# Optimization experiments

Hardware: AMD Instinct MI355X
Metric: run time of the kernel (lower is better)

## Reference

```python
import jax, jax.numpy as jnp
import numpy as np

B, C, H, W = 16, 512, 32, 32
CQ = C // 8  # 64
EPS = 1e-5


def _conv1x1(x, Wt, b=None):
    # x: (B,C,H,W), Wt: (O,C) -> (B,O,H,W)
    y = jnp.einsum('bchw,oc->bohw', x, Wt)
    if b is not None:
        y = y + b[None, :, None, None]
    return y


def setup_inputs() -> dict:
    key = jax.random.key(0)
    ks = jax.random.split(key, 12)
    s = 0.02
    return {
        'rgb':    jax.random.normal(ks[0], (B, C, H, W), jnp.float32),
        'depth':  jax.random.normal(ks[1], (B, C, H, W), jnp.float32),
        'Wq_rgb': jax.random.normal(ks[2], (CQ, C), jnp.float32) * s,
        'bq_rgb': jnp.zeros((CQ,), jnp.float32),
        'Wk_dep': jax.random.normal(ks[3], (CQ, C), jnp.float32) * s,
        'bk_dep': jnp.zeros((CQ,), jnp.float32),
        'Wv_dep': jax.random.normal(ks[4], (C, C), jnp.float32) * s,
        'bv_dep': jnp.zeros((C,), jnp.float32),
        'Wq_dep': jax.random.normal(ks[5], (CQ, C), jnp.float32) * s,
        'bq_dep': jnp.zeros((CQ,), jnp.float32),
        'Wk_rgb': jax.random.normal(ks[6], (CQ, C), jnp.float32) * s,
        'bk_rgb': jnp.zeros((CQ,), jnp.float32),
        'Wv_rgb': jax.random.normal(ks[7], (C, C), jnp.float32) * s,
        'bv_rgb': jnp.zeros((C,), jnp.float32),
        'W_fuse': jax.random.normal(ks[8], (C, 2 * C), jnp.float32) * s,
        'gamma':  jnp.ones((C,), jnp.float32),
        'beta':   jnp.zeros((C,), jnp.float32),
    }


def reference(rgb, depth, Wq_rgb, bq_rgb, Wk_dep, bk_dep, Wv_dep, bv_dep,
              Wq_dep, bq_dep, Wk_rgb, bk_rgb, Wv_rgb, bv_rgb, W_fuse, gamma, beta):
    b, c, h, w = rgb.shape
    hw = h * w
    scale = jnp.asarray(c, rgb.dtype) ** 0.5  # note: full C, as in source

    # RGB attends to depth
    q = _conv1x1(rgb, Wq_rgb, bq_rgb).reshape(b, -1, hw).transpose(0, 2, 1)   # (B,HW,CQ)
    k = _conv1x1(depth, Wk_dep, bk_dep).reshape(b, -1, hw)                    # (B,CQ,HW)
    v = _conv1x1(depth, Wv_dep, bv_dep).reshape(b, -1, hw).transpose(0, 2, 1) # (B,HW,C)
    attn = jax.nn.softmax(jnp.einsum('bnd,bdm->bnm', q, k) / scale, axis=-1)
    rgb_att = jnp.einsum('bnm,bmc->bnc', attn, v).transpose(0, 2, 1).reshape(b, c, h, w)

    # Depth attends to RGB
    q2 = _conv1x1(depth, Wq_dep, bq_dep).reshape(b, -1, hw).transpose(0, 2, 1)
    k2 = _conv1x1(rgb, Wk_rgb, bk_rgb).reshape(b, -1, hw)
    v2 = _conv1x1(rgb, Wv_rgb, bv_rgb).reshape(b, -1, hw).transpose(0, 2, 1)
    attn2 = jax.nn.softmax(jnp.einsum('bnd,bdm->bnm', q2, k2) / scale, axis=-1)
    dep_att = jnp.einsum('bnm,bmc->bnc', attn2, v2).transpose(0, 2, 1).reshape(b, c, h, w)

    cat = jnp.concatenate([rgb_att, dep_att], axis=1)      # (B,2C,H,W)
    fused = jnp.einsum('bchw,oc->bohw', cat, W_fuse)        # 1x1 conv, no bias

    # BatchNorm2d in training mode (batch statistics, biased variance)
    mean = fused.mean(axis=(0, 2, 3))
    var = fused.var(axis=(0, 2, 3))
    normed = (fused - mean[None, :, None, None]) * jax.lax.rsqrt(var + EPS)[None, :, None, None]
    out = normed * gamma[None, :, None, None] + beta[None, :, None, None]
    return jax.nn.relu(out)
```

## Files before the change

kernel.cpp:

```cpp
#include <hip/hip_runtime.h>
#include <math.h>

#define NB 16
#define CC 512
#define CQ 64
#define HWN 1024

typedef float4 f4;
typedef __bf16 bf16x8 __attribute__((ext_vector_type(8)));
typedef float f32x4 __attribute__((ext_vector_type(4)));
typedef __attribute__((ext_vector_type(8))) unsigned short ushort8v;

__device__ __forceinline__ unsigned short f2bf(float f) {
    unsigned int u = __float_as_uint(f);
    u = (u + 0x7fffu + ((u >> 16) & 1u)) >> 16;
    return (unsigned short)u;
}
__device__ __forceinline__ float bf2f(unsigned short u) {
    return __uint_as_float(((unsigned int)u) << 16);
}

__device__ __forceinline__ void gload16(const unsigned short* g, unsigned short* l) {
    __builtin_amdgcn_global_load_lds(
        (const __attribute__((address_space(1))) unsigned int*)g,
        (__attribute__((address_space(3))) unsigned int*)l,
        16, 0, 0);
}

template<int BM, int BN, int BIAS, bool OBF16, int ZSH, bool STATS>
__global__ __launch_bounds__(256)
void mfma_g(const unsigned short* __restrict__ A, long sAlo, long sAhi, int lda,
            const unsigned short* __restrict__ B, long sBlo, long sBhi, int ldb,
            const float* __restrict__ bias, long sBiasHi,
            void* __restrict__ Cout, long sClo, long sChi, int ldc,
            int Ksize, float alpha, float* __restrict__ statsAcc)
{
    constexpr int MF = BM / 32;
    constexpr int NF = BN / 32;
    constexpr int CA = BM / 32;
    constexpr int CB = BN / 32;
    __shared__ unsigned short As[2][BM * 64];
    __shared__ unsigned short Bs[2][BN * 64];

    const int gx = gridDim.x, gy = gridDim.y;
    int f = blockIdx.x + gx * (blockIdx.y + gy * blockIdx.z);
    const int nwg = gx * gy * gridDim.z;
    f = (f & 7) * (nwg >> 3) + (f >> 3);
    const int bx = f % gx; const int t2 = f / gx;
    const int by = t2 % gy; const int bz = t2 / gy;

    const int zlo = ZSH ? (bz & ((1 << ZSH) - 1)) : 0;
    const int zhi = bz >> ZSH;

    const int t = threadIdx.x, lane = t & 63, wid = t >> 6;
    const int wm = (wid >> 1) * (BM / 2), wn = (wid & 1) * (BN / 2);
    const int m0 = by * BM, n0 = bx * BN;
    const unsigned short* Ab = A + (long)zlo * sAlo + (long)zhi * sAhi;
    const unsigned short* Bb = B + (long)zlo * sBlo + (long)zhi * sBhi;

    const int srow = lane >> 3;
    const int scol = ((lane & 7) ^ srow) << 3;
    const unsigned short* gA[CA]; const unsigned short* gB[CB];
    unsigned short* lA[CA]; unsigned short* lB[CB];
#pragma unroll
    for (int c = 0; c < CA; ++c) {
        const int seg = wid + 4 * c;
        gA[c] = Ab + (long)(m0 + seg * 8 + srow) * lda + scol;
        lA[c] = &As[0][seg * 512];
    }
#pragma unroll
    for (int c = 0; c < CB; ++c) {
        const int seg = wid + 4 * c;
        gB[c] = Bb + (long)(n0 + seg * 8 + srow) * ldb + scol;
        lB[c] = &Bs[0][seg * 512];
    }

    f32x4 acc[MF][NF] = {};
    const int l15 = lane & 15, slot = lane >> 4;

#pragma unroll
    for (int c = 0; c < CA; ++c) gload16(gA[c], lA[c]);
#pragma unroll
    for (int c = 0; c < CB; ++c) gload16(gB[c], lB[c]);
    __syncthreads();

    const int nt = Ksize >> 6;
    int cur = 0;
    for (int tt = 0; tt < nt; ++tt) {
        if (tt + 1 < nt) {
            const int ko = (tt + 1) << 6;
            const int nb = cur ^ 1;
#pragma unroll
            for (int c = 0; c < CA; ++c) gload16(gA[c] + ko, lA[c] + nb * (BM * 64));
#pragma unroll
            for (int c = 0; c < CB; ++c) gload16(gB[c] + ko, lB[c] + nb * (BN * 64));
        }
        bf16x8 alo[MF], ahi[MF], blo[NF], bhi[NF];
#pragma unroll
        for (int i = 0; i < MF; ++i) {
            const int r = wm + i * 16 + l15;
            alo[i] = *(const bf16x8*)&As[cur][r * 64 + ((slot ^ (r & 7)) << 3)];
            ahi[i] = *(const bf16x8*)&As[cur][r * 64 + (((slot + 4) ^ (r & 7)) << 3)];
        }
#pragma unroll
        for (int j = 0; j < NF; ++j) {
            const int r = wn + j * 16 + l15;
            blo[j] = *(const bf16x8*)&Bs[cur][r * 64 + ((slot ^ (r & 7)) << 3)];
            bhi[j] = *(const bf16x8*)&Bs[cur][r * 64 + (((slot + 4) ^ (r & 7)) << 3)];
        }
#pragma unroll
        for (int i = 0; i < MF; ++i)
#pragma unroll
            for (int j = 0; j < NF; ++j) {
                acc[i][j] = __builtin_amdgcn_mfma_f32_16x16x32_bf16(alo[i], blo[j], acc[i][j], 0, 0, 0);
                acc[i][j] = __builtin_amdgcn_mfma_f32_16x16x32_bf16(ahi[i], bhi[j], acc[i][j], 0, 0, 0);
            }
        __syncthreads();
        cur ^= 1;
    }

    unsigned short* C16 = (unsigned short*)Cout + (long)zlo * sClo + (long)zhi * sChi;
    float*          C32 = (float*)Cout + (long)zlo * sClo + (long)zhi * sChi;
    const float* biasb = (BIAS != 0) ? bias + (long)zhi * sBiasHi : nullptr;
    const int r0 = slot << 2;
#pragma unroll
    for (int i = 0; i < MF; ++i) {
#pragma unroll
        for (int r = 0; r < 4; ++r) {
            const int m = m0 + wm + i * 16 + r0 + r;
            const float brow = (BIAS == 1) ? biasb[m] : 0.0f;
            float ps = 0.0f, ps2 = 0.0f;
#pragma unroll
            for (int j = 0; j < NF; ++j) {
                const int n = n0 + wn + j * 16 + l15;
                const float bb = (BIAS == 2) ? biasb[n] : brow;
                const float o = alpha * (acc[i][j][r] + bb);
                if (OBF16) C16[(long)m * ldc + n] = f2bf(o);
                else       C32[(long)m * ldc + n] = o;
                if (STATS) { ps += o; ps2 += o * o; }
            }
            if (STATS) {
#pragma unroll
                for (int off = 8; off; off >>= 1) {
                    ps  += __shfl_xor(ps, off);
                    ps2 += __shfl_xor(ps2, off);
                }
                if (l15 == 0) {
                    const int slot2 = ((zlo * gx + bx) << 1) + (wid & 1);
                    statsAcc[(long)m * 256 + slot2]          = ps;
                    statsAcc[131072 + (long)m * 256 + slot2] = ps2;
                }
            }
        }
    }
}

__global__ __launch_bounds__(256)
void attn_fused2(const unsigned short* __restrict__ QK, unsigned short* __restrict__ Pcat)
{
    __shared__ unsigned short Es[16 * 1024];
    const int t = threadIdx.x, lane = t & 63, w = t >> 6;
    const int bx = blockIdx.x, b = blockIdx.y, dir = blockIdx.z;
    const unsigned short* Q = QK + (long)(dir ? b : 16 + b) * 131072;
    const unsigned short* K = QK + (long)(dir ? 16 + b : b) * 131072 + 64;
    const int l15 = lane & 15, slot = lane >> 4, kg = slot << 3;

    const long mrow = (long)bx * 16 + l15;
    bf16x8 aq0 = *(const bf16x8*)&Q[mrow * 128 + kg];
    bf16x8 aq1 = *(const bf16x8*)&Q[mrow * 128 + 32 + kg];

    const int colbase = w << 8;
    const int rbase = slot << 2;
#pragma unroll
    for (int c = 0; c < 4; ++c) {
        const int n0 = colbase + (c << 6);
        bf16x8 bk0[4], bk1[4];
#pragma unroll
        for (int j = 0; j < 4; ++j) {
            const long krow = n0 + (j << 4) + l15;
            bk0[j] = *(const bf16x8*)&K[krow * 128 + kg];
            bk1[j] = *(const bf16x8*)&K[krow * 128 + 32 + kg];
        }
#pragma unroll
        for (int j = 0; j < 4; ++j) {
            f32x4 a = {0.f, 0.f, 0.f, 0.f};
            a = __builtin_amdgcn_mfma_f32_16x16x32_bf16(aq0, bk0[j], a, 0, 0, 0);
            a = __builtin_amdgcn_mfma_f32_16x16x32_bf16(aq1, bk1[j], a, 0, 0, 0);
            const int col = n0 + (j << 4) + l15;
#pragma unroll
            for (int r = 0; r < 4; ++r) {
                const int row = rbase + r;
                Es[(row << 10) + (col ^ (row << 3))] = f2bf(__expf(a[r]));
            }
        }
    }
    __syncthreads();

#pragma unroll
    for (int rr = 0; rr < 4; ++rr) {
        const int R = (w << 2) + rr;
        const int base = R << 10, sw = R << 3;
        const int c8 = lane << 3;
        ushort8v u0 = *(const ushort8v*)&Es[base + (c8 ^ sw)];
        ushort8v u1 = *(const ushort8v*)&Es[base + ((c8 + 512) ^ sw)];
        float v[16];
#pragma unroll
        for (int i = 0; i < 8; ++i) { v[i] = bf2f(u0[i]); v[8 + i] = bf2f(u1[i]); }
        float s = 0.0f;
#pragma unroll
        for (int i = 0; i < 16; ++i) s += v[i];
#pragma unroll
        for (int off = 32; off; off >>= 1) s += __shfl_xor(s, off);
        const float inv = 1.0f / s;
        ushort8v o0, o1;
#pragma unroll
        for (int i = 0; i < 8; ++i) { o0[i] = f2bf(v[i] * inv); o1[i] = f2bf(v[8 + i] * inv); }
        unsigned short* dst = Pcat + ((long)(b * 1024 + bx * 16 + R)) * 2048
                            + dir * 1024 + c8;
        *(ushort8v*)dst = o0;
        *(ushort8v*)(dst + 512) = o1;
    }
}

__global__ __launch_bounds__(256)
void transpose_cvt2(const float* __restrict__ src_dep, const float* __restrict__ src_rgb,
                    unsigned short* __restrict__ dst)
{
    __shared__ float tile[64][65];
    const int t = threadIdx.x;
    const int z = blockIdx.z;
    const float* s = (z < 16 ? src_dep : src_rgb) + (long)(z & 15) * 524288;
    unsigned short* d = dst + (long)z * 524288;
    const int c0 = blockIdx.x << 6, r0 = blockIdx.y << 6;
    const int lr = t >> 4, lc = (t & 15) << 2;
#pragma unroll
    for (int i = 0; i < 4; ++i) {
        f4 v = *(const f4*)(s + (long)(r0 + lr + i * 16) * HWN + c0 + lc);
        *(f4*)&tile[lr + i * 16][lc] = v;
    }
    __syncthreads();
#pragma unroll
    for (int i = 0; i < 4; ++i) {
        const int crow = lr + i * 16;
        ushort4 o;
        o.x = f2bf(tile[lc + 0][crow]);
        o.y = f2bf(tile[lc + 1][crow]);
        o.z = f2bf(tile[lc + 2][crow]);
        o.w = f2bf(tile[lc + 3][crow]);
        *(ushort4*)&d[(long)(c0 + crow) * CC + r0 + lc] = o;
    }
}

__global__ __launch_bounds__(256)
void transpose_cvt(const float* __restrict__ src, unsigned short* __restrict__ dst,
                   int R, int Cn)
{
    __shared__ float tile[64][65];
    const int t = threadIdx.x;
    const int c0 = blockIdx.x << 6, r0 = blockIdx.y << 6;
    const int lr = t >> 4, lc = (t & 15) << 2;
#pragma unroll
    for (int i = 0; i < 4; ++i) {
        f4 v = *(const f4*)(src + (long)(r0 + lr + i * 16) * Cn + c0 + lc);
        *(f4*)&tile[lr + i * 16][lc] = v;
    }
    __syncthreads();
#pragma unroll
    for (int i = 0; i < 4; ++i) {
        const int crow = lr + i * 16;
        ushort4 o;
        o.x = f2bf(tile[lc + 0][crow]);
        o.y = f2bf(tile[lc + 1][crow]);
        o.z = f2bf(tile[lc + 2][crow]);
        o.w = f2bf(tile[lc + 3][crow]);
        *(ushort4*)&dst[(long)(c0 + crow) * R + r0 + lc] = o;
    }
}

__global__ __launch_bounds__(256)
void cvt_flat(const float* __restrict__ src, unsigned short* __restrict__ dst, int n4)
{
    const int i = blockIdx.x * 256 + threadIdx.x;
    if (i < n4) {
        f4 v = ((const f4*)src)[i];
        ushort4 o;
        o.x = f2bf(v.x); o.y = f2bf(v.y); o.z = f2bf(v.z); o.w = f2bf(v.w);
        ((ushort4*)dst)[i] = o;
    }
}

__global__ __launch_bounds__(256)
void prep_wqk(const float* __restrict__ wqd, const float* __restrict__ wkd,
              const float* __restrict__ wqr, const float* __restrict__ wkr,
              unsigned short* __restrict__ dst, float s)
{
    const int i4 = blockIdx.x * 256 + threadIdx.x;
    const int row = i4 >> 7;
    const int seg = row >> 6;
    const float* src = (seg == 0) ? wqd : (seg == 1) ? wkd : (seg == 2) ? wqr : wkr;
    const float sc = (seg & 1) ? 1.0f : s;
    f4 v = ((const f4*)src)[((row & 63) << 7) + (i4 & 127)];
    ushort4 o;
    o.x = f2bf(v.x * sc); o.y = f2bf(v.y * sc); o.z = f2bf(v.z * sc); o.w = f2bf(v.w * sc);
    ((ushort4*)dst)[i4] = o;
}

__global__ __launch_bounds__(256)
void prep_bias(const float* __restrict__ bqd, const float* __restrict__ bkd,
               const float* __restrict__ bqr, const float* __restrict__ bkr,
               float* __restrict__ dst, float s)
{
    const int t = threadIdx.x;
    float v;
    if (t < 64)       v = bqd[t] * s;
    else if (t < 128) v = bkd[t - 64];
    else if (t < 192) v = bqr[t - 128] * s;
    else              v = bkr[t - 192];
    dst[t] = v;
}

__global__ __launch_bounds__(256)
void bfuse_k(const float* __restrict__ Wf, const float* __restrict__ bv1,
             const float* __restrict__ bv2, float* __restrict__ bfuse)
{
    const int o = blockIdx.x, t = threadIdx.x;
    const float* row = Wf + (long)o * 1024;
    float s = row[t] * bv1[t] + row[512 + t] * bv2[t]
            + row[256 + t] * bv1[256 + t] + row[768 + t] * bv2[256 + t];
#pragma unroll
    for (int off = 32; off; off >>= 1) s += __shfl_xor(s, off);
    __shared__ float r[4];
    if ((t & 63) == 0) r[t >> 6] = s;
    __syncthreads();
    if (t == 0) bfuse[o] = r[0] + r[1] + r[2] + r[3];
}

__global__ __launch_bounds__(256)
void bn_finalize(const float* __restrict__ part, float* __restrict__ stats)
{
    const int c = blockIdx.x, t = threadIdx.x;
    float s1 = part[(long)c * 256 + t];
    float s2 = part[131072 + (long)c * 256 + t];
#pragma unroll
    for (int off = 32; off; off >>= 1) {
        s1 += __shfl_xor(s1, off);
        s2 += __shfl_xor(s2, off);
    }
    __shared__ float r1[4], r2[4];
    if ((t & 63) == 0) { r1[t >> 6] = s1; r2[t >> 6] = s2; }
    __syncthreads();
    if (t == 0) {
        const float S1 = r1[0] + r1[1] + r1[2] + r1[3];
        const float S2 = r2[0] + r2[1] + r2[2] + r2[3];
        const float mean = S1 * (1.0f / 16384.0f);
        const float var  = S2 * (1.0f / 16384.0f) - mean * mean;
        stats[c]      = mean;
        stats[CC + c] = rsqrtf(var + 1e-5f);
    }
}

__global__ __launch_bounds__(256)
void bn_apply(const float* __restrict__ fused, const float* __restrict__ stats,
              const float* __restrict__ gamma, const float* __restrict__ beta,
              float* __restrict__ out)
{
    const long i4 = (long)blockIdx.x * 256 + threadIdx.x;
    f4 v = ((const f4*)fused)[i4];
    const int o = (int)((i4 >> 8) & 511);
    const float is = stats[CC + o];
    const float g  = gamma[o] * is;
    const float bb = beta[o] - stats[o] * g;
    v.x = fmaxf(fmaf(v.x, g, bb), 0.0f);
    v.y = fmaxf(fmaf(v.y, g, bb), 0.0f);
    v.z = fmaxf(fmaf(v.z, g, bb), 0.0f);
    v.w = fmaxf(fmaf(v.w, g, bb), 0.0f);
    ((f4*)out)[i4] = v;
}

static constexpr long B_depT  = 0;
static constexpr long B_rgbT  = 16777216;
static constexpr long B_WvT1  = 33554432;
static constexpr long B_WvT2  = 34078720;
static constexpr long B_Wfb   = 34603008;
static constexpr long B_Wqk   = 35651584;
static constexpr long B_Wc1   = 35913728;
static constexpr long B_bfu   = 36962304;
static constexpr long B_bias  = 36964352;
static constexpr long B_QK    = 36966400;
static constexpr long B_Acat  = 45355008;
static constexpr long B_Pcat  = 78909440;
static constexpr long B_fused = 146018304;
static constexpr long B_stats = 179572736;
static constexpr long B_part  = 179576832;

extern "C" void kernel_launch(void* const* d_in, const int* in_sizes, int n_in,
                              void* d_out, int out_size, void* d_ws, size_t ws_size,
                              hipStream_t stream)
{
    const float* rgb    = (const float*)d_in[0];
    const float* depth  = (const float*)d_in[1];
    const float* Wq_rgb = (const float*)d_in[2];
    const float* bq_rgb = (const float*)d_in[3];
    const float* Wk_dep = (const float*)d_in[4];
    const float* bk_dep = (const float*)d_in[5];
    const float* Wv_dep = (const float*)d_in[6];
    const float* bv_dep = (const float*)d_in[7];
    const float* Wq_dep = (const float*)d_in[8];
    const float* bq_dep = (const float*)d_in[9];
    const float* Wk_rgb = (const float*)d_in[10];
    const float* bk_rgb = (const float*)d_in[11];
    const float* Wv_rgb = (const float*)d_in[12];
    const float* bv_rgb = (const float*)d_in[13];
    const float* W_fuse = (const float*)d_in[14];
    const float* gamma  = (const float*)d_in[15];
    const float* beta   = (const float*)d_in[16];
    char* ws = (char*)d_ws;
    float* out = (float*)d_out;

    const float inv_scale = 0.044194173824159223f;
    dim3 blk(256);

    unsigned short* depT = (unsigned short*)(ws + B_depT);
    unsigned short* WvT1 = (unsigned short*)(ws + B_WvT1);
    unsigned short* WvT2 = (unsigned short*)(ws + B_WvT2);
    unsigned short* Wfb  = (unsigned short*)(ws + B_Wfb);
    unsigned short* Wqk  = (unsigned short*)(ws + B_Wqk);
    unsigned short* Wc1  = (unsigned short*)(ws + B_Wc1);
    float*          bfu  = (float*)(ws + B_bfu);
    float*          bias = (float*)(ws + B_bias);
    unsigned short* QK   = (unsigned short*)(ws + B_QK);
    unsigned short* Acat = (unsigned short*)(ws + B_Acat);
    unsigned short* Pcat = (unsigned short*)(ws + B_Pcat);
    float*          fused= (float*)(ws + B_fused);
    float*          stats= (float*)(ws + B_stats);
    float*          part = (float*)(ws + B_part);

    transpose_cvt2<<<dim3(16, 8, 32), blk, 0, stream>>>(depth, rgb, depT);
    transpose_cvt<<<dim3(8, 8, 1), blk, 0, stream>>>(Wv_dep, WvT1, CC, CC);
    transpose_cvt<<<dim3(8, 8, 1), blk, 0, stream>>>(Wv_rgb, WvT2, CC, CC);
    cvt_flat<<<512, blk, 0, stream>>>(W_fuse, Wfb, 131072);
    prep_wqk<<<128, blk, 0, stream>>>(Wq_dep, Wk_dep, Wq_rgb, Wk_rgb, Wqk, inv_scale);
    prep_bias<<<1, blk, 0, stream>>>(bq_dep, bk_dep, bq_rgb, bk_rgb, bias, inv_scale);
    bfuse_k<<<512, blk, 0, stream>>>(W_fuse, bv_dep, bv_rgb, bfu);

    mfma_g<128, 128, 0, true, 0, false><<<dim3(4, 4, 2), blk, 0, stream>>>(
        Wfb, 0, 512, 1024, WvT1, 0, 262144, 512, nullptr, 0,
        Wc1, 0, 262144, 512, 512, 1.0f, nullptr);

    mfma_g<128, 64, 2, true, 4, false><<<dim3(2, 8, 32), blk, 0, stream>>>(
        depT, 524288, 8388608, 512, Wqk, 0, 65536, 512, bias, 128,
        QK, 131072, 2097152, 128, 512, 1.0f, nullptr);

    mfma_g<128, 128, 0, true, 4, false><<<dim3(8, 4, 32), blk, 0, stream>>>(
        Wc1, 0, 262144, 512, depT, 524288, 8388608, 512, nullptr, 0,
        Acat, 1048576, 1024, 2048, 512, 1.0f, nullptr);

    attn_fused2<<<dim3(64, NB, 2), blk, 0, stream>>>(QK, Pcat);

    mfma_g<128, 128, 1, false, 4, true><<<dim3(8, 4, 16), blk, 0, stream>>>(
        Acat, 1048576, 0, 2048, Pcat, 2097152, 0, 2048, bfu, 0,
        fused, 524288, 0, 1024, 2048, 1.0f, part);

    bn_finalize<<<512, blk, 0, stream>>>(part, stats);
    bn_apply<<<8192, blk, 0, stream>>>(fused, stats, gamma, beta, out);
}
```

Baseline: 175.5 us.

## Store fused output as bf16, merge weight transposes, remap attention blocks, widen QK tile

The fused 1x1-conv output is now written in bf16 instead of fp32, and the BN apply kernel reads it as bf16. This halves the traffic for that intermediate write and read. The two Wv transposes become one launch, the attention grid is remapped so consecutive blocks are spread across XCD-like groups, and the QK projection GEMM uses a 128-wide N tile. BN statistics still come from the fp32 partial sums, but the normalized values are computed from bf16-rounded data, which adds precision error.

```diff
diff --git a/kernel.cpp b/kernel.cpp
--- a/kernel.cpp
+++ b/kernel.cpp
@@ -160,7 +160,9 @@
 {
     __shared__ unsigned short Es[16 * 1024];
     const int t = threadIdx.x, lane = t & 63, w = t >> 6;
-    const int bx = blockIdx.x, b = blockIdx.y, dir = blockIdx.z;
+    int p = blockIdx.x + 64 * (blockIdx.y + 16 * blockIdx.z);
+    p = (p & 7) * 256 + (p >> 3);
+    const int bx = p & 63, b = (p >> 6) & 15, dir = p >> 10;
     const unsigned short* Q = QK + (long)(dir ? b : 16 + b) * 131072;
     const unsigned short* K = QK + (long)(dir ? 16 + b : b) * 131072 + 64;
     const int l15 = lane & 15, slot = lane >> 4, kg = slot << 3;
@@ -252,16 +254,19 @@
 }
 
 __global__ __launch_bounds__(256)
-void transpose_cvt(const float* __restrict__ src, unsigned short* __restrict__ dst,
-                   int R, int Cn)
+void transpose_cvtW(const float* __restrict__ w0, const float* __restrict__ w1,
+                    unsigned short* __restrict__ dst)
 {
     __shared__ float tile[64][65];
     const int t = threadIdx.x;
+    const int z = blockIdx.z;
+    const float* src = z ? w1 : w0;
+    unsigned short* d = dst + (long)z * 262144;
     const int c0 = blockIdx.x << 6, r0 = blockIdx.y << 6;
     const int lr = t >> 4, lc = (t & 15) << 2;
 #pragma unroll
     for (int i = 0; i < 4; ++i) {
-        f4 v = *(const f4*)(src + (long)(r0 + lr + i * 16) * Cn + c0 + lc);
+        f4 v = *(const f4*)(src + (long)(r0 + lr + i * 16) * CC + c0 + lc);
         *(f4*)&tile[lr + i * 16][lc] = v;
     }
     __syncthreads();
@@ -273,7 +278,7 @@
         o.y = f2bf(tile[lc + 1][crow]);
         o.z = f2bf(tile[lc + 2][crow]);
         o.w = f2bf(tile[lc + 3][crow]);
-        *(ushort4*)&dst[(long)(c0 + crow) * R + r0 + lc] = o;
+        *(ushort4*)&d[(long)(c0 + crow) * CC + r0 + lc] = o;
     }
 }
 
@@ -360,27 +365,32 @@
 }
 
 __global__ __launch_bounds__(256)
-void bn_apply(const float* __restrict__ fused, const float* __restrict__ stats,
-              const float* __restrict__ gamma, const float* __restrict__ beta,
-              float* __restrict__ out)
-{
-    const long i4 = (long)blockIdx.x * 256 + threadIdx.x;
-    f4 v = ((const f4*)fused)[i4];
-    const int o = (int)((i4 >> 8) & 511);
+void bn_apply_bf16(const unsigned short* __restrict__ fused, const float* __restrict__ stats,
+                   const float* __restrict__ gamma, const float* __restrict__ beta,
+                   float* __restrict__ out)
+{
+    const long i8 = (long)blockIdx.x * 256 + threadIdx.x;
+    ushort8v v = ((const ushort8v*)fused)[i8];
+    const int o = (int)((i8 >> 7) & 511);
     const float is = stats[CC + o];
     const float g  = gamma[o] * is;
     const float bb = beta[o] - stats[o] * g;
-    v.x = fmaxf(fmaf(v.x, g, bb), 0.0f);
-    v.y = fmaxf(fmaf(v.y, g, bb), 0.0f);
-    v.z = fmaxf(fmaf(v.z, g, bb), 0.0f);
-    v.w = fmaxf(fmaf(v.w, g, bb), 0.0f);
-    ((f4*)out)[i4] = v;
+    f4 o0, o1;
+    o0.x = fmaxf(fmaf(bf2f(v[0]), g, bb), 0.0f);
+    o0.y = fmaxf(fmaf(bf2f(v[1]), g, bb), 0.0f);
+    o0.z = fmaxf(fmaf(bf2f(v[2]), g, bb), 0.0f);
+    o0.w = fmaxf(fmaf(bf2f(v[3]), g, bb), 0.0f);
+    o1.x = fmaxf(fmaf(bf2f(v[4]), g, bb), 0.0f);
+    o1.y = fmaxf(fmaf(bf2f(v[5]), g, bb), 0.0f);
+    o1.z = fmaxf(fmaf(bf2f(v[6]), g, bb), 0.0f);
+    o1.w = fmaxf(fmaf(bf2f(v[7]), g, bb), 0.0f);
+    ((f4*)out)[i8 * 2]     = o0;
+    ((f4*)out)[i8 * 2 + 1] = o1;
 }
 
 static constexpr long B_depT  = 0;
 static constexpr long B_rgbT  = 16777216;
 static constexpr long B_WvT1  = 33554432;
-static constexpr long B_WvT2  = 34078720;
 static constexpr long B_Wfb   = 34603008;
 static constexpr long B_Wqk   = 35651584;
 static constexpr long B_Wc1   = 35913728;
@@ -422,7 +432,6 @@
 
     unsigned short* depT = (unsigned short*)(ws + B_depT);
     unsigned short* WvT1 = (unsigned short*)(ws + B_WvT1);
-    unsigned short* WvT2 = (unsigned short*)(ws + B_WvT2);
     unsigned short* Wfb  = (unsigned short*)(ws + B_Wfb);
     unsigned short* Wqk  = (unsigned short*)(ws + B_Wqk);
     unsigned short* Wc1  = (unsigned short*)(ws + B_Wc1);
@@ -431,13 +440,12 @@
     unsigned short* QK   = (unsigned short*)(ws + B_QK);
     unsigned short* Acat = (unsigned short*)(ws + B_Acat);
     unsigned short* Pcat = (unsigned short*)(ws + B_Pcat);
-    float*          fused= (float*)(ws + B_fused);
+    unsigned short* fused= (unsigned short*)(ws + B_fused);
     float*          stats= (float*)(ws + B_stats);
     float*          part = (float*)(ws + B_part);
 
     transpose_cvt2<<<dim3(16, 8, 32), blk, 0, stream>>>(depth, rgb, depT);
-    transpose_cvt<<<dim3(8, 8, 1), blk, 0, stream>>>(Wv_dep, WvT1, CC, CC);
-    transpose_cvt<<<dim3(8, 8, 1), blk, 0, stream>>>(Wv_rgb, WvT2, CC, CC);
+    transpose_cvtW<<<dim3(8, 8, 2), blk, 0, stream>>>(Wv_dep, Wv_rgb, WvT1);
     cvt_flat<<<512, blk, 0, stream>>>(W_fuse, Wfb, 131072);
     prep_wqk<<<128, blk, 0, stream>>>(Wq_dep, Wk_dep, Wq_rgb, Wk_rgb, Wqk, inv_scale);
     prep_bias<<<1, blk, 0, stream>>>(bq_dep, bk_dep, bq_rgb, bk_rgb, bias, inv_scale);
@@ -447,7 +455,7 @@
         Wfb, 0, 512, 1024, WvT1, 0, 262144, 512, nullptr, 0,
         Wc1, 0, 262144, 512, 512, 1.0f, nullptr);
 
-    mfma_g<128, 64, 2, true, 4, false><<<dim3(2, 8, 32), blk, 0, stream>>>(
+    mfma_g<128, 128, 2, true, 4, false><<<dim3(1, 8, 32), blk, 0, stream>>>(
         depT, 524288, 8388608, 512, Wqk, 0, 65536, 512, bias, 128,
         QK, 131072, 2097152, 128, 512, 1.0f, nullptr);
 
@@ -457,10 +465,10 @@
 
     attn_fused2<<<dim3(64, NB, 2), blk, 0, stream>>>(QK, Pcat);
 
-    mfma_g<128, 128, 1, false, 4, true><<<dim3(8, 4, 16), blk, 0, stream>>>(
+    mfma_g<128, 128, 1, true, 4, true><<<dim3(8, 4, 16), blk, 0, stream>>>(
         Acat, 1048576, 0, 2048, Pcat, 2097152, 0, 2048, bfu, 0,
         fused, 524288, 0, 1024, 2048, 1.0f, part);
 
     bn_finalize<<<512, blk, 0, stream>>>(part, stats);
-    bn_apply<<<8192, blk, 0, stream>>>(fused, stats, gamma, beta, out);
-}
+    bn_apply_bf16<<<4096, blk, 0, stream>>>(fused, stats, gamma, beta, out);
+}
```

Measured after the change: 175.3 us. Within noise of the previous version (-0.1%).
